# Kernel optimization log

Measured on AMD Instinct MI355X. Metric: run time of the kernel, lower is better.

The kernel has to match this reference:

```python
import jax, jax.numpy as jnp
import numpy as np

N_VARS = 32        # n_variables
TEMPERATURE = 1.0  # softmax temperature (default)


def setup_inputs() -> dict:
    key = jax.random.key(0)
    k1, k2 = jax.random.split(key)
    B, C, T = 16, 3072, 2048  # C = n_var * (hidden_dim + n_var) = 32*(64+32)
    x = jax.random.normal(k1, (B, C, T), dtype=jnp.float32)
    x_instant = jax.random.normal(k2, (B, C, T), dtype=jnp.float32)
    return {"x": x, "x_instant": x_instant}


def _split_context_attention(v, n):
    B, _, T = v.shape
    v = v.reshape(B, n, -1, T)          # (B, n, hidden+n, T)
    attn = v[:, :, :n, :]               # (B, n, n, T) attention logits
    ctx = v[:, :, n:, :]                # (B, n, hidden, T)
    return ctx, attn


def reference(x, x_instant):
    n = N_VARS
    B, _, T = x.shape
    ctx, attn = _split_context_attention(x, n)
    ctx_i, attn_i = _split_context_attention(x_instant, n)
    ctx = jnp.concatenate([ctx, ctx_i], axis=-3)     # (B, 2n, hidden, T)
    attn = jnp.concatenate([attn, attn_i], axis=-2)  # (B, n, 2n, T)
    attn = jax.nn.softmax(attn / TEMPERATURE, axis=-2)
    # aggregate contexts with attention weights
    out = jnp.einsum('bijt,bjdt->bidt', attn, ctx)   # (B, n, hidden, T)
    out = out.reshape(B, -1, T)                      # (B, n*hidden, T)
    # ConvertInstant: zero the instantaneous self-edge (j = n + i), then sum chunks
    a1 = attn[:, :, :n, :]
    a2 = attn[:, :, n:, :]
    diag = jnp.eye(n, dtype=bool)[None, :, :, None]  # (1, n, n, 1)
    a2 = jnp.where(diag, jnp.zeros((), dtype=attn.dtype), a2)
    attentions = a1 + a2                             # (B, n, n, T)
    return out, attentions
```

## Files before the change

### kernel.cpp

```cpp
#include <hip/hip_runtime.h>
#include <stdint.h>


typedef unsigned int uint_t;
typedef float  f32x4   __attribute__((ext_vector_type(4)));
typedef short  short8v __attribute__((ext_vector_type(8)));

constexpr int Bq = 16, Cq = 3072, Tq = 2048;
constexpr int TT = 32, TILES = 64, NBLK = Bq * TILES;
constexpr size_t ATT_OFF = (size_t)Bq * 2048 * Tq;
constexpr int TBS = 4224;
constexpr int LDS_BYTES = 135168;

__global__ __launch_bounds__(1024, 1) void attn_v12(const float* __restrict__ x,
                                                    const float* __restrict__ xi,
                                                    float* __restrict__ out)
{
    __shared__ __align__(16) unsigned char smem[LDS_BYTES];
    unsigned short* LU = (unsigned short*)smem;
    uint_t*         LW = (uint_t*)smem;
    float*          LF = (float*)smem;

    const int tid  = (int)threadIdx.x;
    const int b    = (int)blockIdx.x >> 6;
    const int tile = (int)blockIdx.x & (TILES - 1);
    const int t0   = tile * TT;
    const int tl   = tid & 31;
    const int slot = tid >> 5;

    const float* xb  = x  + (size_t)b * Cq * Tq + t0 + tl;
    const float* xib = xi + (size_t)b * Cq * Tq + t0 + tl;

    uint_t pk[32];
    {
        const int i = slot;
        float p[64];
#pragma unroll
        for (int j = 0; j < 32; ++j) p[j]      = xb [(size_t)(i * 96 + j) * Tq];
#pragma unroll
        for (int j = 0; j < 32; ++j) p[j + 32] = xib[(size_t)(i * 96 + j) * Tq];
        float m = p[0];
#pragma unroll
        for (int j = 1; j < 64; ++j) m = fmaxf(m, p[j]);
        float s = 0.f;
#pragma unroll
        for (int j = 0; j < 64; ++j) { p[j] = __expf(p[j] - m); s += p[j]; }
        const float inv = 1.f / s;
#pragma unroll
        for (int j = 0; j < 64; ++j) p[j] *= inv;

        float* ao = out + ATT_OFF + ((size_t)(b * 32 + i) * 32) * Tq + t0 + tl;
#pragma unroll
        for (int j = 0; j < 32; ++j) {
            float v = p[j] + ((j == i) ? 0.f : p[j + 32]);
            __builtin_nontemporal_store(v, &ao[(size_t)j * Tq]);
        }
#pragma unroll
        for (int k = 0; k < 32; ++k) {
            uint_t b0 = __float_as_uint(p[2 * k]);
            uint_t b1 = __float_as_uint(p[2 * k + 1]);
            uint_t lo = (b0 + 0x7fffu + ((b0 >> 16) & 1u)) >> 16;
            uint_t hi = (b1 + 0x7fffu + ((b1 >> 16) & 1u)) >> 16;
            pk[k] = lo | (hi << 16);
        }
    }

    const int fw  = ((slot >> 2) & 3) ^ (slot & 3);
    const int TBw = tl * TBS + (tl & 7) * 16;

    const int l   = tid & 63;
    const int wv  = tid >> 6;
    const int frd = ((l >> 2) & 3) ^ (l & 3);
    const int kbr = (((l >> 4) ^ frd) & 3) * 16;
    const int rA  = (l & 15) * 64;

#pragma unroll
    for (int dh = 0; dh < 2; ++dh) {
        f32x4 acc[2][2][2];
#pragma unroll
        for (int q = 0; q < 2; ++q)
#pragma unroll
            for (int s = 0; s < 2; ++s)
#pragma unroll
                for (int dt = 0; dt < 2; ++dt) acc[q][s][dt] = (f32x4)(0.f);

#pragma unroll
        for (int jh = 0; jh < 2; ++jh) {
#pragma unroll
            for (int m = 0; m < 16; ++m) {
                const int kbx  = (m >> 2) ^ fw;
                const int byte = TBw + slot * 64 + kbx * 16 + ((2 * m) & 7) * 2;
                LW[byte >> 2] = pk[jh * 16 + m];
            }
            {
                const float* src = (jh == 0) ? x : xi;
                const float* sp  = src + (size_t)b * Cq * Tq
                                 + (size_t)(32 + dh * 32 + slot) * Tq + t0 + tl;
#pragma unroll 8
                for (int kk = 0; kk < 32; ++kk) {
                    const float v = sp[(size_t)kk * 96 * Tq];
                    const uint_t bb = __float_as_uint(v);
                    const unsigned short h =
                        (unsigned short)((bb + 0x7fffu + ((bb >> 16) & 1u)) >> 16);
                    const int kbx  = (kk >> 3) ^ fw;
                    const int byte = TBw + 2048 + slot * 64 + kbx * 16 + (kk & 7) * 2;
                    LU[byte >> 1] = h;
                }
            }
            __syncthreads();

#pragma unroll
            for (int q = 0; q < 2; ++q) {
                const int tloc = 2 * wv + q;
                const int base = tloc * TBS + (tloc & 7) * 16;
                const short8v A0 = *(const short8v*)(smem + base        + rA + kbr);
                const short8v A1 = *(const short8v*)(smem + base + 1024 + rA + kbr);
                const short8v B0 = *(const short8v*)(smem + base + 2048 + rA + kbr);
                const short8v B1 = *(const short8v*)(smem + base + 3072 + rA + kbr);
                acc[q][0][0] = __builtin_amdgcn_mfma_f32_16x16x32_bf16(A0, B0, acc[q][0][0], 0, 0, 0);
                acc[q][0][1] = __builtin_amdgcn_mfma_f32_16x16x32_bf16(A0, B1, acc[q][0][1], 0, 0, 0);
                acc[q][1][0] = __builtin_amdgcn_mfma_f32_16x16x32_bf16(A1, B0, acc[q][1][0], 0, 0, 0);
                acc[q][1][1] = __builtin_amdgcn_mfma_f32_16x16x32_bf16(A1, B1, acc[q][1][1], 0, 0, 0);
            }
            __syncthreads();
        }

#pragma unroll
        for (int q = 0; q < 2; ++q)
#pragma unroll
            for (int s = 0; s < 2; ++s)
#pragma unroll
                for (int dt = 0; dt < 2; ++dt)
#pragma unroll
                    for (int ri = 0; ri < 4; ++ri) {
                        const int ii = s * 16 + (l >> 4) * 4 + ri;
                        const int dl = dt * 16 + (l & 15);
                        LF[(ii * 32 + dl) * 33 + 2 * wv + q] = acc[q][s][dt][ri];
                    }
        __syncthreads();
        {
            float* ob = out + (size_t)b * 2048 * Tq + t0 + tl;
#pragma unroll 8
            for (int kk = 0; kk < 32; ++kk) {
                const int ch = kk * 64 + dh * 32 + slot;
                __builtin_nontemporal_store(LF[(kk * 32 + slot) * 33 + tl],
                                            &ob[(size_t)ch * Tq]);
            }
        }
        __syncthreads();
    }
}

extern "C" void kernel_launch(void* const* d_in, const int* in_sizes, int n_in,
                              void* d_out, int out_size, void* d_ws, size_t ws_size,
                              hipStream_t stream) {
    const float* x  = (const float*)d_in[0];
    const float* xi = (const float*)d_in[1];
    float* out = (float*)d_out;
    attn_v12<<<dim3(NBLK), dim3(1024), 0, stream>>>(x, xi, out);
}
```

Baseline: 270.8 us.

## Prefetch next context chunk into registers while MFMA runs on current chunk

Context loads from global memory are restructured into a software pipeline: the next chunk's 32 floats are loaded into registers before the current chunk's MFMA work, so global latency overlaps compute and LDS staging. LDS staging writes are also widened, with paired bf16 values packed into 32-bit stores and pk pairs into 64-bit stores. This raises register pressure with 32 extra live floats per thread at 1024 threads per block, which may risk spills.

```diff
diff --git a/kernel.cpp b/kernel.cpp
--- a/kernel.cpp
+++ b/kernel.cpp
@@ -12,14 +12,14 @@
 constexpr int TBS = 4224;
 constexpr int LDS_BYTES = 135168;
 
-__global__ __launch_bounds__(1024, 1) void attn_v12(const float* __restrict__ x,
+__global__ __launch_bounds__(1024, 1) void attn_v13(const float* __restrict__ x,
                                                     const float* __restrict__ xi,
                                                     float* __restrict__ out)
 {
     __shared__ __align__(16) unsigned char smem[LDS_BYTES];
-    unsigned short* LU = (unsigned short*)smem;
-    uint_t*         LW = (uint_t*)smem;
-    float*          LF = (float*)smem;
+    uint_t*    LW = (uint_t*)smem;
+    uint64_t*  LQ = (uint64_t*)smem;
+    float*     LF = (float*)smem;
 
     const int tid  = (int)threadIdx.x;
     const int b    = (int)blockIdx.x >> 6;
@@ -32,6 +32,17 @@
     const float* xib = xi + (size_t)b * Cq * Tq + t0 + tl;
 
     uint_t pk[32];
+    float  cre[32];
+
+    auto issue = [&](int c) {
+        const int dh = c >> 1, jh = c & 1;
+        const float* src = (jh == 0) ? x : xi;
+        const float* sp  = src + (size_t)b * Cq * Tq
+                         + (size_t)(32 + dh * 32 + slot) * Tq + t0 + tl;
+#pragma unroll
+        for (int kk = 0; kk < 32; ++kk) cre[kk] = sp[(size_t)kk * 96 * Tq];
+    };
+
     {
         const int i = slot;
         float p[64];
@@ -64,6 +75,7 @@
             pk[k] = lo | (hi << 16);
         }
     }
+    issue(0);
 
     const int fw  = ((slot >> 2) & 3) ^ (slot & 3);
     const int TBw = tl * TBS + (tl & 7) * 16;
@@ -74,57 +86,54 @@
     const int kbr = (((l >> 4) ^ frd) & 3) * 16;
     const int rA  = (l & 15) * 64;
 
+    auto stageP = [&](int jh) {
 #pragma unroll
-    for (int dh = 0; dh < 2; ++dh) {
-        f32x4 acc[2][2][2];
+        for (int m = 0; m < 16; m += 2) {
+            const int kbx  = (m >> 2) ^ fw;
+            const int byte = TBw + slot * 64 + kbx * 16 + ((2 * m) & 7) * 2;
+            uint64_t w = (uint64_t)pk[jh * 16 + m] |
+                         ((uint64_t)pk[jh * 16 + m + 1] << 32);
+            LQ[byte >> 3] = w;
+        }
+    };
+    auto stageC = [&]() {
+#pragma unroll
+        for (int kk = 0; kk < 32; kk += 2) {
+            uint_t b0 = __float_as_uint(cre[kk]);
+            uint_t b1 = __float_as_uint(cre[kk + 1]);
+            uint_t h0 = (b0 + 0x7fffu + ((b0 >> 16) & 1u)) >> 16;
+            uint_t h1 = (b1 + 0x7fffu + ((b1 >> 16) & 1u)) >> 16;
+            const int kbx  = (kk >> 3) ^ fw;
+            const int byte = TBw + 2048 + slot * 64 + kbx * 16 + (kk & 7) * 2;
+            LW[byte >> 2] = h0 | (h1 << 16);
+        }
+    };
+
+    f32x4 acc[2][2][2];
+    auto accClr = [&]() {
 #pragma unroll
         for (int q = 0; q < 2; ++q)
 #pragma unroll
             for (int s = 0; s < 2; ++s)
 #pragma unroll
                 for (int dt = 0; dt < 2; ++dt) acc[q][s][dt] = (f32x4)(0.f);
-
+    };
+    auto mfmaChunk = [&]() {
 #pragma unroll
-        for (int jh = 0; jh < 2; ++jh) {
-#pragma unroll
-            for (int m = 0; m < 16; ++m) {
-                const int kbx  = (m >> 2) ^ fw;
-                const int byte = TBw + slot * 64 + kbx * 16 + ((2 * m) & 7) * 2;
-                LW[byte >> 2] = pk[jh * 16 + m];
-            }
-            {
-                const float* src = (jh == 0) ? x : xi;
-                const float* sp  = src + (size_t)b * Cq * Tq
-                                 + (size_t)(32 + dh * 32 + slot) * Tq + t0 + tl;
-#pragma unroll 8
-                for (int kk = 0; kk < 32; ++kk) {
-                    const float v = sp[(size_t)kk * 96 * Tq];
-                    const uint_t bb = __float_as_uint(v);
-                    const unsigned short h =
-                        (unsigned short)((bb + 0x7fffu + ((bb >> 16) & 1u)) >> 16);
-                    const int kbx  = (kk >> 3) ^ fw;
-                    const int byte = TBw + 2048 + slot * 64 + kbx * 16 + (kk & 7) * 2;
-                    LU[byte >> 1] = h;
-                }
-            }
-            __syncthreads();
-
-#pragma unroll
-            for (int q = 0; q < 2; ++q) {
-                const int tloc = 2 * wv + q;
-                const int base = tloc * TBS + (tloc & 7) * 16;
-                const short8v A0 = *(const short8v*)(smem + base        + rA + kbr);
-                const short8v A1 = *(const short8v*)(smem + base + 1024 + rA + kbr);
-                const short8v B0 = *(const short8v*)(smem + base + 2048 + rA + kbr);
-                const short8v B1 = *(const short8v*)(smem + base + 3072 + rA + kbr);
-                acc[q][0][0] = __builtin_amdgcn_mfma_f32_16x16x32_bf16(A0, B0, acc[q][0][0], 0, 0, 0);
-                acc[q][0][1] = __builtin_amdgcn_mfma_f32_16x16x32_bf16(A0, B1, acc[q][0][1], 0, 0, 0);
-                acc[q][1][0] = __builtin_amdgcn_mfma_f32_16x16x32_bf16(A1, B0, acc[q][1][0], 0, 0, 0);
-                acc[q][1][1] = __builtin_amdgcn_mfma_f32_16x16x32_bf16(A1, B1, acc[q][1][1], 0, 0, 0);
-            }
-            __syncthreads();
+        for (int q = 0; q < 2; ++q) {
+            const int tloc = 2 * wv + q;
+            const int base = tloc * TBS + (tloc & 7) * 16;
+            const short8v A0 = *(const short8v*)(smem + base        + rA + kbr);
+            const short8v A1 = *(const short8v*)(smem + base + 1024 + rA + kbr);
+            const short8v B0 = *(const short8v*)(smem + base + 2048 + rA + kbr);
+            const short8v B1 = *(const short8v*)(smem + base + 3072 + rA + kbr);
+            acc[q][0][0] = __builtin_amdgcn_mfma_f32_16x16x32_bf16(A0, B0, acc[q][0][0], 0, 0, 0);
+            acc[q][0][1] = __builtin_amdgcn_mfma_f32_16x16x32_bf16(A0, B1, acc[q][0][1], 0, 0, 0);
+            acc[q][1][0] = __builtin_amdgcn_mfma_f32_16x16x32_bf16(A1, B0, acc[q][1][0], 0, 0, 0);
+            acc[q][1][1] = __builtin_amdgcn_mfma_f32_16x16x32_bf16(A1, B1, acc[q][1][1], 0, 0, 0);
         }
-
+    };
+    auto dump = [&](int dh) {
 #pragma unroll
         for (int q = 0; q < 2; ++q)
 #pragma unroll
@@ -138,17 +147,39 @@
                         LF[(ii * 32 + dl) * 33 + 2 * wv + q] = acc[q][s][dt][ri];
                     }
         __syncthreads();
-        {
-            float* ob = out + (size_t)b * 2048 * Tq + t0 + tl;
+        float* ob = out + (size_t)b * 2048 * Tq + t0 + tl;
 #pragma unroll 8
-            for (int kk = 0; kk < 32; ++kk) {
-                const int ch = kk * 64 + dh * 32 + slot;
-                __builtin_nontemporal_store(LF[(kk * 32 + slot) * 33 + tl],
-                                            &ob[(size_t)ch * Tq]);
-            }
+        for (int kk = 0; kk < 32; ++kk) {
+            const int ch = kk * 64 + dh * 32 + slot;
+            __builtin_nontemporal_store(LF[(kk * 32 + slot) * 33 + tl],
+                                        &ob[(size_t)ch * Tq]);
         }
         __syncthreads();
-    }
+    };
+
+    accClr();
+    stageP(0); stageC();
+    __syncthreads();
+    issue(1);
+    mfmaChunk();
+    __syncthreads();
+    stageP(1); stageC();
+    __syncthreads();
+    issue(2);
+    mfmaChunk();
+    __syncthreads();
+    dump(0);
+    accClr();
+    stageP(0); stageC();
+    __syncthreads();
+    issue(3);
+    mfmaChunk();
+    __syncthreads();
+    stageP(1); stageC();
+    __syncthreads();
+    mfmaChunk();
+    __syncthreads();
+    dump(1);
 }
 
 extern "C" void kernel_launch(void* const* d_in, const int* in_sizes, int n_in,
@@ -157,5 +188,5 @@
     const float* x  = (const float*)d_in[0];
     const float* xi = (const float*)d_in[1];
     float* out = (float*)d_out;
-    attn_v12<<<dim3(NBLK), dim3(1024), 0, stream>>>(x, xi, out);
+    attn_v13<<<dim3(NBLK), dim3(1024), 0, stream>>>(x, xi, out);
 }
```

New measurement: 258.6 us. -4.5%, faster.
